# Performance work log

Measured on AMD Instinct MI355X. Metric: run time of the kernel, lower is better.

Reference implementation:

```python
import jax, jax.numpy as jnp
import numpy as np

TEMP = 0.1
GAMMA = 0.75
CHUNK = 300      # hardcoded b=300 in the original forward
EPS = 1e-8
LOSS_WEIGHT = 0.1


def _l2norm(x, axis):
    return x / (jnp.linalg.norm(x, axis=axis, keepdims=True) + 1e-12)


def setup_inputs() -> dict:
    key = jax.random.key(0)
    k = jax.random.split(key, 6)
    B, D, C = 2, 128, 19
    H = W = 240          # full image -> n = 57600 negatives (192 chunks of 300)
    h = w = 60           # overlap crop size -> P = 3600 anchor pixels
    feats_view1 = _l2norm(jax.random.normal(k[0], (B, D, H, W), jnp.float32), axis=1)
    pos_feats1 = _l2norm(jax.random.normal(k[1], (B, D, h, w), jnp.float32), axis=1)
    pos_feats2 = _l2norm(jax.random.normal(k[2], (B, D, h, w), jnp.float32), axis=1)
    pseudo_logits1 = jax.random.uniform(k[3], (B, C, h, w), jnp.float32)
    pseudo_logits2 = jax.random.uniform(k[4], (B, C, h, w), jnp.float32)
    neg_pseudo_logits = jax.random.uniform(k[5], (B, C, H, W), jnp.float32)
    return {
        "feats_view1": feats_view1,
        "pos_feats1": pos_feats1,
        "pos_feats2": pos_feats2,
        "pseudo_logits1": pseudo_logits1,
        "pseudo_logits2": pseudo_logits2,
        "neg_pseudo_logits": neg_pseudo_logits,
    }


def _per_sample(f1, f2, nf, pl1, pl2, npl):
    # f1,f2: [D,h,w] cropped overlap feats; nf: [D,H,W] negatives; pl*: [C,h,w]; npl: [C,H,W]
    D = f1.shape[0]
    C = pl1.shape[0]
    feats1 = f1.reshape(D, -1)                               # [D, P]
    feats2 = jax.lax.stop_gradient(f2.reshape(D, -1))        # detach() in original
    P = feats1.shape[1]
    neg_feats = nf.reshape(D, -1)                            # [D, N]
    N = neg_feats.shape[1]
    labels1 = jnp.argmax(pl1.reshape(C, -1), axis=0)         # [P] anchor pseudo-labels
    neg_labels = jnp.argmax(npl.reshape(C, -1), axis=0)      # [N] negative pseudo-labels

    pos1 = (feats1 * feats2).sum(0) / TEMP                   # [P]

    nchunks = N // CHUNK                                     # N chosen divisible by CHUNK
    nf_c = neg_feats.reshape(D, nchunks, CHUNK).transpose(1, 0, 2)  # [K, D, b]
    nl_c = neg_labels.reshape(nchunks, CHUNK)                       # [K, b]

    def step(acc, xs):
        nfi, nli = xs
        scores = jnp.einsum('dp,db->pb', feats1, nfi) / TEMP        # [P, b]
        mask = (labels1[:, None] != nli[None, :]).astype(scores.dtype)
        return acc + (mask * jnp.exp(scores)).sum(-1), None

    neg_logits, _ = jax.lax.scan(step, jnp.zeros((P,), feats1.dtype), (nf_c, nl_c))

    pos_exp = jnp.exp(pos1)
    lossn = -jnp.log(pos_exp / (pos_exp + neg_logits + EPS) + EPS)  # [P]

    # mask1 = argmax over classes of (dir_mask * pos_mask), as in the original
    combo = ((pl1 < pl2) & (pl2 > GAMMA)).astype(lossn.dtype).reshape(C, -1)
    mask1 = jnp.argmax(combo, axis=0).astype(lossn.dtype)           # [P]
    return (mask1 * lossn).sum() / (mask1.sum() + EPS)


def reference(feats_view1, pos_feats1, pos_feats2, pseudo_logits1, pseudo_logits2, neg_pseudo_logits):
    losses = jax.vmap(_per_sample)(pos_feats1, pos_feats2, feats_view1,
                                   pseudo_logits1, pseudo_logits2, neg_pseudo_logits)
    return LOSS_WEIGHT * (losses[0] + losses[1])
```

## Files before the change

### kernel.cpp

```cpp
#include <hip/hip_runtime.h>
#include <string.h>

#define D_ 128
#define P_ 3600
#define N_ 57600
#define C_ 19
#define NB 2
#define NSPLIT 30
#define CHPB 15
#define PT 29

typedef short bf16x8 __attribute__((ext_vector_type(8)));
typedef float f32x4 __attribute__((ext_vector_type(4)));

__device__ __forceinline__ ushort f2bf(float x) {
  unsigned u = __float_as_uint(x);
  u = (u + 0x7fffu + ((u >> 16) & 1u)) >> 16;
  return (ushort)u;
}

__device__ __forceinline__ void gload_lds16(const void* g, void* l) {
  __builtin_amdgcn_global_load_lds(
      (const __attribute__((address_space(1))) unsigned int*)g,
      (__attribute__((address_space(3))) unsigned int*)l, 16, 0, 0);
}

__global__ void prep_kernel(const float* __restrict__ XB, ushort* __restrict__ YB,
                            const float* __restrict__ XA, ushort* __restrict__ YA,
                            const float* __restrict__ npl, int* __restrict__ nlab,
                            const float* __restrict__ pl1, const float* __restrict__ pl2,
                            const float* __restrict__ f2,
                            int* __restrict__ lab1, float* __restrict__ mask1,
                            float* __restrict__ pos1, float* __restrict__ neg_logits) {
  __shared__ float T[64][129];
  const int b = blockIdx.y;
  const int tid = threadIdx.x;

  if (blockIdx.x >= N_ / 64 + 57) {
    int p = (blockIdx.x - (N_ / 64 + 57)) * 256 + tid;
    if (p >= P_) return;
    const float* a1 = pl1 + (size_t)b * C_ * P_ + p;
    const float* a2 = pl2 + (size_t)b * C_ * P_ + p;
    float best = a1[0]; int bi = 0;
    int mfirst = ((a1[0] < a2[0]) && (a2[0] > 0.75f)) ? 0 : -1;
#pragma unroll
    for (int c = 1; c < C_; ++c) {
      float v1 = a1[(size_t)c * P_], v2 = a2[(size_t)c * P_];
      if (v1 > best) { best = v1; bi = c; }
      if (mfirst < 0 && (v1 < v2) && (v2 > 0.75f)) mfirst = c;
    }
    lab1[b * P_ + p] = bi;
    mask1[b * P_ + p] = (mfirst < 0) ? 0.0f : (float)mfirst;
    neg_logits[b * P_ + p] = 0.0f;
    const float* g1 = XA + (size_t)b * D_ * P_ + p;
    const float* g2 = f2 + (size_t)b * D_ * P_ + p;
    float s = 0.f;
#pragma unroll 8
    for (int d = 0; d < D_; ++d) s += g1[(size_t)d * P_] * g2[(size_t)d * P_];
    pos1[b * P_ + p] = s * 10.0f;
    return;
  }

  const bool isB = blockIdx.x < (N_ / 64);
  const int M = isB ? N_ : P_;
  const float scale = isB ? 1.0f : 14.4269504089f;
  const int nbase = (isB ? blockIdx.x : (blockIdx.x - N_ / 64)) * 64;
  const float* Xb = (isB ? XB : XA) + (size_t)b * D_ * M;
  ushort* Yb = (isB ? YB : YA) + (size_t)b * M * D_;
  const int nl = tid & 63;
  const int dw = tid >> 6;
#pragma unroll
  for (int i = 0; i < 32; ++i) {
    int d = i * 4 + dw;
    int gn = nbase + nl; if (gn >= M) gn = M - 1;
    T[nl][d] = Xb[(size_t)d * M + gn];
  }
  __syncthreads();
  const int d0 = (tid & 31) * 4;
#pragma unroll
  for (int i = 0; i < 8; ++i) {
    int n = i * 8 + (tid >> 5);
    int gn = nbase + n;
    if (gn < M) {
      ushort4 u;
      u.x = f2bf(T[n][d0 + 0] * scale);
      u.y = f2bf(T[n][d0 + 1] * scale);
      u.z = f2bf(T[n][d0 + 2] * scale);
      u.w = f2bf(T[n][d0 + 3] * scale);
      *(ushort4*)(Yb + (size_t)gn * D_ + d0) = u;
    }
  }
  if (isB && tid < 64) {
    int gn = nbase + tid;
    const float* base = npl + (size_t)b * C_ * N_ + gn;
    float best = base[0]; int bi = 0;
#pragma unroll
    for (int c = 1; c < C_; ++c) {
      float v = base[(size_t)c * N_];
      if (v > best) { best = v; bi = c; }
    }
    nlab[b * N_ + gn] = bi;
  }
}

__global__ __launch_bounds__(256, 2) void gemm_kernel(
    const ushort* __restrict__ At, const ushort* __restrict__ Bt,
    const int* __restrict__ lab1g, const int* __restrict__ nlabg,
    float* __restrict__ neg_logits) {
  __shared__ __attribute__((aligned(16))) ushort Bs[2][128 * 128];
  const int flat = blockIdx.x;
  const int xcd = flat & 7;
  const int rem = flat >> 3;
  const int slot = rem / PT;
  const int ptile = rem % PT;
  const int g = slot * 8 + xcd;
  if (g >= 2 * NSPLIT) return;
  const int y = g >> 1;
  const int b = g & 1;

  const int tid = threadIdx.x;
  const int wid = tid >> 6, lane = tid & 63;
  const int quad = lane >> 4, lm = lane & 15;
  const int qr = wid & 1, qc = wid >> 1;
  const ushort* Atb = At + (size_t)b * P_ * D_;
  const ushort* Btb = Bt + (size_t)b * N_ * D_;
  const int* lab1 = lab1g + b * P_;
  const int* nlab = nlabg + b * N_;

  const int row4 = wid * 4 + (lane >> 4);
  const int cc = lane & 15;
  const int swz = cc ^ (row4 & 7);

#pragma unroll
  for (int i = 0; i < 8; ++i) {
    int row = i * 16 + row4;
    int p = ptile * 128 + row; if (p > P_ - 1) p = P_ - 1;
    gload_lds16(Atb + (size_t)p * D_ + swz * 8, &Bs[0][(i * 16 + wid * 4) * 128]);
  }
  __syncthreads();

  bf16x8 af[4][4];
#pragma unroll
  for (int r = 0; r < 4; ++r) {
    int row = qr * 64 + r * 16 + lm;
#pragma unroll
    for (int k0 = 0; k0 < 4; ++k0) {
      int ch = (k0 * 4 + quad) ^ (row & 7);
      af[r][k0] = *(const bf16x8*)(&Bs[0][row * 128 + ch * 8]);
    }
  }

  int labp[16];
#pragma unroll
  for (int r = 0; r < 4; ++r)
#pragma unroll
    for (int gg = 0; gg < 4; ++gg) {
      int p = ptile * 128 + qr * 64 + r * 16 + quad * 4 + gg;
      labp[r * 4 + gg] = lab1[p > P_ - 1 ? P_ - 1 : p];
    }

  float rsum[16];
#pragma unroll
  for (int i = 0; i < 16; ++i) rsum[i] = 0.f;
  const f32x4 zero4 = {0.f, 0.f, 0.f, 0.f};

  const int c0 = y * CHPB;
  const int c1 = c0 + CHPB;
  const ushort* srcB = Btb + (size_t)row4 * D_ + swz * 8;

  __syncthreads();
  {
    const ushort* s = srcB + (size_t)c0 * 128 * D_;
#pragma unroll
    for (int i = 0; i < 8; ++i)
      gload_lds16(s + (size_t)i * 16 * D_, &Bs[0][(i * 16 + wid * 4) * 128]);
  }

  for (int j = c0; j < c1; ++j) {
    const int p = (j - c0) & 1;
    const int nbase = j * 128;
    __syncthreads();
    if (j + 1 < c1) {
      const ushort* s = srcB + (size_t)(j + 1) * 128 * D_;
#pragma unroll
      for (int i = 0; i < 8; ++i)
        gload_lds16(s + (size_t)i * 16 * D_, &Bs[p ^ 1][(i * 16 + wid * 4) * 128]);
    }

#pragma unroll
    for (int c = 0; c < 4; ++c) {
      const int row = qc * 64 + c * 16 + lm;
      const int nl = nlab[nbase + row];
      f32x4 acc[4];
      {
        int ch = quad ^ (row & 7);
        bf16x8 bf = *(const bf16x8*)(&Bs[p][row * 128 + ch * 8]);
#pragma unroll
        for (int r = 0; r < 4; ++r)
          acc[r] = __builtin_amdgcn_mfma_f32_16x16x32_bf16(af[r][0], bf, zero4, 0, 0, 0);
      }
#pragma unroll
      for (int k0 = 1; k0 < 4; ++k0) {
        int ch = (k0 * 4 + quad) ^ (row & 7);
        bf16x8 bf = *(const bf16x8*)(&Bs[p][row * 128 + ch * 8]);
#pragma unroll
        for (int r = 0; r < 4; ++r)
          acc[r] = __builtin_amdgcn_mfma_f32_16x16x32_bf16(af[r][k0], bf, acc[r], 0, 0, 0);
      }
#pragma unroll
      for (int r = 0; r < 4; ++r)
#pragma unroll
        for (int gg = 0; gg < 4; ++gg) {
          float e = __builtin_amdgcn_exp2f(acc[r][gg]);
          rsum[r * 4 + gg] += (labp[r * 4 + gg] != nl) ? e : 0.f;
        }
    }
  }

#pragma unroll
  for (int i = 0; i < 16; ++i) {
    float v = rsum[i];
    v += __shfl_xor(v, 1);
    v += __shfl_xor(v, 2);
    v += __shfl_xor(v, 4);
    v += __shfl_xor(v, 8);
    rsum[i] = v;
  }
  if (lm == 0) {
#pragma unroll
    for (int r = 0; r < 4; ++r)
#pragma unroll
      for (int gg = 0; gg < 4; ++gg) {
        int p = ptile * 128 + qr * 64 + r * 16 + quad * 4 + gg;
        if (p < P_) atomicAdd(&neg_logits[b * P_ + p], rsum[r * 4 + gg]);
      }
  }
}

__global__ void finalize_kernel(const float* __restrict__ neg_logits,
                                const float* __restrict__ pos1,
                                const float* __restrict__ mask1,
                                float* __restrict__ out) {
  double s1[2] = {0.0, 0.0}, s2[2] = {0.0, 0.0};
  for (int idx = threadIdx.x; idx < NB * P_; idx += 256) {
    int b = idx / P_;
    float ne = neg_logits[idx];
    float pe = __expf(pos1[idx]);
    float l = -logf(pe / (pe + ne + 1e-8f) + 1e-8f);
    float w = mask1[idx];
    s1[b] += (double)(w * l);
    s2[b] += (double)w;
  }
#pragma unroll
  for (int off = 32; off > 0; off >>= 1) {
    s1[0] += __shfl_down(s1[0], off);
    s2[0] += __shfl_down(s2[0], off);
    s1[1] += __shfl_down(s1[1], off);
    s2[1] += __shfl_down(s2[1], off);
  }
  __shared__ double sm[4][4];
  int wid = threadIdx.x >> 6, lane = threadIdx.x & 63;
  if (lane == 0) { sm[wid][0] = s1[0]; sm[wid][1] = s2[0]; sm[wid][2] = s1[1]; sm[wid][3] = s2[1]; }
  __syncthreads();
  if (threadIdx.x == 0) {
    double a = 0, bsum = 0, c = 0, d = 0;
    for (int w = 0; w < 4; ++w) { a += sm[w][0]; bsum += sm[w][1]; c += sm[w][2]; d += sm[w][3]; }
    out[0] = (float)(0.1 * (a / (bsum + 1e-8) + c / (d + 1e-8)));
  }
}

extern "C" void kernel_launch(void* const* d_in, const int* in_sizes, int n_in,
                              void* d_out, int out_size, void* d_ws, size_t ws_size,
                              hipStream_t stream) {
  const float* feats_view1 = (const float*)d_in[0];
  const float* pos_feats1  = (const float*)d_in[1];
  const float* pos_feats2  = (const float*)d_in[2];
  const float* pl1 = (const float*)d_in[3];
  const float* pl2 = (const float*)d_in[4];
  const float* npl = (const float*)d_in[5];

  char* ws = (char*)d_ws;
  ushort* Bt        = (ushort*)(ws + 0);
  ushort* At        = (ushort*)(ws + 29491200);
  int*    nlab      = (int*)   (ws + 31334400);
  int*    lab1      = (int*)   (ws + 31795200);
  float*  mask1     = (float*) (ws + 31824000);
  float*  pos1      = (float*) (ws + 31852800);
  float*  neg_logits= (float*) (ws + 31881600);

  prep_kernel<<<dim3(N_ / 64 + 57 + 15, NB), 256, 0, stream>>>(
      feats_view1, Bt, pos_feats1, At, npl, nlab,
      pl1, pl2, pos_feats2, lab1, mask1, pos1, neg_logits);
  gemm_kernel<<<dim3(8 * PT * 8), 256, 0, stream>>>(At, Bt, lab1, nlab, neg_logits);
  finalize_kernel<<<1, 256, 0, stream>>>(neg_logits, pos1, mask1, (float*)d_out);
}
```

Baseline: 274.7 us.

## Halve GEMM LDS tiles to 64 rows, raise occupancy, rebalance N-split, vectorize prep loads

The GEMM kernel now streams negatives in 64-row half-tiles with a smaller double-buffered LDS array. This lets launch bounds ask for 3 blocks per CU instead of 2, and the N dimension is split into 26 uneven ranges over 450 chunks to rebalance the grid. The prep kernel's transpose load now uses float4 global reads instead of scalar ones. The trade-offs are more barriers per unit of work, tighter register budgets at higher occupancy, and more LDS bank conflicts on the transposed stores.

```diff
diff --git a/kernel.cpp b/kernel.cpp
--- a/kernel.cpp
+++ b/kernel.cpp
@@ -6,8 +6,8 @@
 #define N_ 57600
 #define C_ 19
 #define NB 2
-#define NSPLIT 30
-#define CHPB 15
+#define NSPLIT 26
+#define TOTCH 450
 #define PT 29
 
 typedef short bf16x8 __attribute__((ext_vector_type(8)));
@@ -67,13 +67,18 @@
   const int nbase = (isB ? blockIdx.x : (blockIdx.x - N_ / 64)) * 64;
   const float* Xb = (isB ? XB : XA) + (size_t)b * D_ * M;
   ushort* Yb = (isB ? YB : YA) + (size_t)b * M * D_;
-  const int nl = tid & 63;
-  const int dw = tid >> 6;
-#pragma unroll
-  for (int i = 0; i < 32; ++i) {
-    int d = i * 4 + dw;
-    int gn = nbase + nl; if (gn >= M) gn = M - 1;
-    T[nl][d] = Xb[(size_t)d * M + gn];
+  const int nq = tid & 15;
+  const int dr = tid >> 4;
+#pragma unroll
+  for (int i = 0; i < 8; ++i) {
+    int d = i * 16 + dr;
+    int gn0 = nbase + nq * 4;
+    if (gn0 > M - 4) gn0 = M - 4;
+    float4 v = *(const float4*)(Xb + (size_t)d * M + gn0);
+    T[nq * 4 + 0][d] = v.x;
+    T[nq * 4 + 1][d] = v.y;
+    T[nq * 4 + 2][d] = v.z;
+    T[nq * 4 + 3][d] = v.w;
   }
   __syncthreads();
   const int d0 = (tid & 31) * 4;
@@ -103,11 +108,11 @@
   }
 }
 
-__global__ __launch_bounds__(256, 2) void gemm_kernel(
+__global__ __launch_bounds__(256, 3) void gemm_kernel(
     const ushort* __restrict__ At, const ushort* __restrict__ Bt,
     const int* __restrict__ lab1g, const int* __restrict__ nlabg,
     float* __restrict__ neg_logits) {
-  __shared__ __attribute__((aligned(16))) ushort Bs[2][128 * 128];
+  __shared__ __attribute__((aligned(16))) ushort Sh[2][64 * 128];
   const int flat = blockIdx.x;
   const int xcd = flat & 7;
   const int rem = flat >> 3;
@@ -127,7 +132,7 @@
   const int* lab1 = lab1g + b * P_;
   const int* nlab = nlabg + b * N_;
 
-  const int row4 = wid * 4 + (lane >> 4);
+  const int row4 = wid * 4 + quad;
   const int cc = lane & 15;
   const int swz = cc ^ (row4 & 7);
 
@@ -135,7 +140,7 @@
   for (int i = 0; i < 8; ++i) {
     int row = i * 16 + row4;
     int p = ptile * 128 + row; if (p > P_ - 1) p = P_ - 1;
-    gload_lds16(Atb + (size_t)p * D_ + swz * 8, &Bs[0][(i * 16 + wid * 4) * 128]);
+    gload_lds16(Atb + (size_t)p * D_ + swz * 8, &Sh[0][0] + (i * 16 + wid * 4) * 128);
   }
   __syncthreads();
 
@@ -146,7 +151,7 @@
 #pragma unroll
     for (int k0 = 0; k0 < 4; ++k0) {
       int ch = (k0 * 4 + quad) ^ (row & 7);
-      af[r][k0] = *(const bf16x8*)(&Bs[0][row * 128 + ch * 8]);
+      af[r][k0] = *(const bf16x8*)(&Sh[0][0] + row * 128 + ch * 8);
     }
   }
 
@@ -164,45 +169,43 @@
   for (int i = 0; i < 16; ++i) rsum[i] = 0.f;
   const f32x4 zero4 = {0.f, 0.f, 0.f, 0.f};
 
-  const int c0 = y * CHPB;
-  const int c1 = c0 + CHPB;
-  const ushort* srcB = Btb + (size_t)row4 * D_ + swz * 8;
-
-  __syncthreads();
-  {
-    const ushort* s = srcB + (size_t)c0 * 128 * D_;
-#pragma unroll
-    for (int i = 0; i < 8; ++i)
-      gload_lds16(s + (size_t)i * 16 * D_, &Bs[0][(i * 16 + wid * 4) * 128]);
-  }
-
-  for (int j = c0; j < c1; ++j) {
-    const int p = (j - c0) & 1;
-    const int nbase = j * 128;
+  const int c0 = (y * TOTCH) / NSPLIT;
+  const int c1 = ((y + 1) * TOTCH) / NSPLIT;
+  const int Hh = (c1 - c0) * 2;
+  const ushort* srcB = Btb + (size_t)(c0 * 128 + row4) * D_ + swz * 8;
+
+  __syncthreads();
+#pragma unroll
+  for (int i = 0; i < 4; ++i)
+    gload_lds16(srcB + (size_t)(i * 16) * D_, &Sh[0][(i * 16 + wid * 4) * 128]);
+
+  for (int t = 0; t < Hh; ++t) {
+    const int buf = t & 1;
     __syncthreads();
-    if (j + 1 < c1) {
-      const ushort* s = srcB + (size_t)(j + 1) * 128 * D_;
-#pragma unroll
-      for (int i = 0; i < 8; ++i)
-        gload_lds16(s + (size_t)i * 16 * D_, &Bs[p ^ 1][(i * 16 + wid * 4) * 128]);
-    }
-
-#pragma unroll
-    for (int c = 0; c < 4; ++c) {
-      const int row = qc * 64 + c * 16 + lm;
-      const int nl = nlab[nbase + row];
+    if (t + 1 < Hh) {
+      const ushort* s = srcB + (size_t)((t + 1) * 64) * D_;
+#pragma unroll
+      for (int i = 0; i < 4; ++i)
+        gload_lds16(s + (size_t)(i * 16) * D_, &Sh[buf ^ 1][(i * 16 + wid * 4) * 128]);
+    }
+
+    const int nb64 = c0 * 128 + t * 64;
+#pragma unroll
+    for (int c = 0; c < 2; ++c) {
+      const int brow = qc * 32 + c * 16 + lm;
+      const int nl = nlab[nb64 + brow];
       f32x4 acc[4];
       {
-        int ch = quad ^ (row & 7);
-        bf16x8 bf = *(const bf16x8*)(&Bs[p][row * 128 + ch * 8]);
+        int ch = quad ^ (lm & 7);
+        bf16x8 bf = *(const bf16x8*)(&Sh[buf][brow * 128 + ch * 8]);
 #pragma unroll
         for (int r = 0; r < 4; ++r)
           acc[r] = __builtin_amdgcn_mfma_f32_16x16x32_bf16(af[r][0], bf, zero4, 0, 0, 0);
       }
 #pragma unroll
       for (int k0 = 1; k0 < 4; ++k0) {
-        int ch = (k0 * 4 + quad) ^ (row & 7);
-        bf16x8 bf = *(const bf16x8*)(&Bs[p][row * 128 + ch * 8]);
+        int ch = (k0 * 4 + quad) ^ (lm & 7);
+        bf16x8 bf = *(const bf16x8*)(&Sh[buf][brow * 128 + ch * 8]);
 #pragma unroll
         for (int r = 0; r < 4; ++r)
           acc[r] = __builtin_amdgcn_mfma_f32_16x16x32_bf16(af[r][k0], bf, acc[r], 0, 0, 0);
@@ -291,6 +294,6 @@
   prep_kernel<<<dim3(N_ / 64 + 57 + 15, NB), 256, 0, stream>>>(
       feats_view1, Bt, pos_feats1, At, npl, nlab,
       pl1, pl2, pos_feats2, lab1, mask1, pos1, neg_logits);
-  gemm_kernel<<<dim3(8 * PT * 8), 256, 0, stream>>>(At, Bt, lab1, nlab, neg_logits);
+  gemm_kernel<<<dim3(8 * 7 * PT), 256, 0, stream>>>(At, Bt, lab1, nlab, neg_logits);
   finalize_kernel<<<1, 256, 0, stream>>>(neg_logits, pos1, mask1, (float*)d_out);
 }
```

New measurement: 270.7 us. No clear change (-1.5%).
